# Kernel optimization log

Hardware: AMD Instinct MI355X
Metric: run time of the kernel (lower is better)

## Reference

```python
import jax, jax.numpy as jnp
import numpy as np

B, N, D = 16, 1024, 768
H = 12
HD = D // H           # 64
NUM_BUCKETS = 49      # iRPE 'product' buckets, shared across heads
SCALE = HD ** -0.5


def setup_inputs() -> dict:
    key = jax.random.key(0)
    k1, k2, k3, k4, k5, k6 = jax.random.split(key, 6)
    x = jax.random.normal(k1, (B, N, D), dtype=jnp.float32)
    qkv_w = jax.random.normal(k2, (3 * D, D), dtype=jnp.float32) * 0.02
    rpe_table = jax.random.normal(k3, (NUM_BUCKETS, HD), dtype=jnp.float32) * 0.02
    rp_bucket = jax.random.randint(k4, (N, N), 0, NUM_BUCKETS, dtype=jnp.int32)
    proj_w = jax.random.normal(k5, (D, D), dtype=jnp.float32) * 0.02
    proj_b = jax.random.normal(k6, (D,), dtype=jnp.float32) * 0.02
    return {"x": x, "qkv_w": qkv_w, "rpe_table": rpe_table,
            "rp_bucket": rp_bucket, "proj_w": proj_w, "proj_b": proj_b}


def reference(x, qkv_w, rpe_table, rp_bucket, proj_w, proj_b):
    b, n, d = x.shape
    # qkv projection (no bias), split into q,k,v of shape [B,H,N,HD]
    qkv = (x @ qkv_w.T).reshape(b, n, 3, H, HD)
    qkv = jnp.transpose(qkv, (2, 0, 3, 1, 4))
    q, k, v = qkv[0], qkv[1], qkv[2]
    q = q * SCALE
    # full attention scores [B,H,N,N]
    attn = jnp.einsum('bhid,bhjd->bhij', q, k)
    # iRPE contextual bias on keys: project q onto the bucket table, then
    # gather per relative-position bucket: bias[b,h,i,j] = (q @ W^T)[b,h,i,rp_bucket[i,j]]
    bias_all = jnp.einsum('bhid,cd->bhic', q, rpe_table)   # [B,H,N,num_buckets]
    bias = bias_all[:, :, jnp.arange(n)[:, None], rp_bucket]  # [B,H,N,N]
    attn = jax.nn.softmax(attn + bias, axis=-1)
    out = jnp.einsum('bhij,bhjd->bhid', attn, v)            # [B,H,N,HD]
    out = jnp.transpose(out, (0, 2, 1, 3)).reshape(b, n, d)
    return out @ proj_w.T + proj_b
```

## Files before the change

### kernel.cpp

```cpp
#include <hip/hip_runtime.h>

typedef short bf16x8 __attribute__((ext_vector_type(8)));
typedef float f32x4 __attribute__((ext_vector_type(4)));

#define QSCALE 0.1803368801111204f

__device__ __forceinline__ unsigned short f2bf(float f){
  unsigned u = __float_as_uint(f);
  u = (u + 0x7fffu + ((u >> 16) & 1u)) >> 16;
  return (unsigned short)u;
}
__device__ __forceinline__ f32x4 mfma16(bf16x8 a, bf16x8 b, f32x4 c){
  return __builtin_amdgcn_mfma_f32_16x16x32_bf16(a, b, c, 0, 0, 0);
}
__device__ __forceinline__ void gload_lds16(const void* g, void* l){
  __builtin_amdgcn_global_load_lds((__attribute__((address_space(1))) void*)(g),
                                   (__attribute__((address_space(3))) void*)(l), 16, 0, 0);
}
__device__ __forceinline__ unsigned cvt_pk_bf16(float lo, float hi){
  unsigned r;
  asm("v_cvt_pk_bf16_f32 %0, %1, %2" : "=v"(r) : "v"(lo), "v"(hi));
  return r;
}
__device__ __forceinline__ float exp2_fast(float x){
  float r;
  asm("v_exp_f32 %0, %1" : "=v"(r) : "v"(x));
  return r;
}

__global__ __launch_bounds__(256) void prep_kernel(
    const float* __restrict__ x, const float* __restrict__ qw,
    const float* __restrict__ pw, const int* __restrict__ rp,
    unsigned short* __restrict__ xb, unsigned short* __restrict__ wb,
    unsigned short* __restrict__ pwb, unsigned char* __restrict__ rp8){
  const int T1 = 3145728;
  const int T2 = T1 + 442368;
  const int T3 = T2 + 147456;
  const int T4 = T3 + 262144;
  for (int t = blockIdx.x * 256 + threadIdx.x; t < T4; t += gridDim.x * 256){
    if (t < T3){
      const float4* src; ushort4* dst; int off;
      if (t < T1){ src = (const float4*)x;  dst = (ushort4*)xb;  off = t; }
      else if (t < T2){ src = (const float4*)qw; dst = (ushort4*)wb;  off = t - T1; }
      else { src = (const float4*)pw; dst = (ushort4*)pwb; off = t - T2; }
      float4 v = src[off];
      ushort4 u;
      u.x = f2bf(v.x); u.y = f2bf(v.y); u.z = f2bf(v.z); u.w = f2bf(v.w);
      dst[off] = u;
    } else {
      int off = t - T3;
      int4 v = ((const int4*)rp)[off];
      int row = (off * 4) >> 10;
      int sw = (row & 7) << 4;
      uchar4 u;
      u.x = (unsigned char)((v.x << 1) ^ sw);
      u.y = (unsigned char)((v.y << 1) ^ sw);
      u.z = (unsigned char)((v.z << 1) ^ sw);
      u.w = (unsigned char)((v.w << 1) ^ sw);
      ((uchar4*)rp8)[off] = u;
    }
  }
}

__device__ __forceinline__ void gemm_core(
    const unsigned short* __restrict__ A, const unsigned short* __restrict__ Bm,
    int m0, int n0, int K, unsigned short* As, unsigned short* Bs,
    f32x4 (&acc)[4][4]){
  const int tid = threadIdx.x, lane = tid & 63, wave = tid >> 6;
  const int g = lane >> 4, r16 = lane & 15;
  const int wr = wave >> 1, wc = wave & 1;
  for (int k0 = 0; k0 < K; k0 += 32){
    __syncthreads();
    #pragma unroll
    for (int j = 0; j < 2; j++){
      int ci = j * 256 + tid;
      int row = ci >> 2, c = ci & 3;
      gload_lds16(A  + (size_t)(m0 + row) * K + k0 + c * 8,
                  (char*)As + (j * 256 + wave * 64) * 16);
      gload_lds16(Bm + (size_t)(n0 + row) * K + k0 + c * 8,
                  (char*)Bs + (j * 256 + wave * 64) * 16);
    }
    __syncthreads();
    bf16x8 a[4], b[4];
    #pragma unroll
    for (int mi = 0; mi < 4; mi++)
      a[mi] = *(const bf16x8*)((const char*)As + (wr * 64 + mi * 16 + r16) * 64 + g * 16);
    #pragma unroll
    for (int ni = 0; ni < 4; ni++)
      b[ni] = *(const bf16x8*)((const char*)Bs + (wc * 64 + ni * 16 + r16) * 64 + g * 16);
    #pragma unroll
    for (int mi = 0; mi < 4; mi++)
      #pragma unroll
      for (int ni = 0; ni < 4; ni++)
        acc[mi][ni] = mfma16(b[ni], a[mi], acc[mi][ni]);
  }
}

__global__ __launch_bounds__(256) void qkv_gemm(
    const unsigned short* __restrict__ xb, const unsigned short* __restrict__ wb,
    unsigned short* __restrict__ q_s, unsigned short* __restrict__ k_s,
    unsigned short* __restrict__ v_t){
  __shared__ __align__(16) unsigned short As[128 * 32];
  __shared__ __align__(16) unsigned short Bs[128 * 32];
  f32x4 acc[4][4];
  #pragma unroll
  for (int i = 0; i < 4; i++)
    #pragma unroll
    for (int j = 0; j < 4; j++){
      acc[i][j][0] = 0.f; acc[i][j][1] = 0.f; acc[i][j][2] = 0.f; acc[i][j][3] = 0.f;
    }
  const int m0 = blockIdx.y * 128, n0 = blockIdx.x * 128;
  gemm_core(xb, wb, m0, n0, 768, As, Bs, acc);

  const int lane = threadIdx.x & 63, wave = threadIdx.x >> 6;
  const int g = lane >> 4, r16 = lane & 15;
  const int wr = wave >> 1, wc = wave & 1;
  const int sel = n0 / 768;
  #pragma unroll
  for (int mi = 0; mi < 4; mi++){
    int grow = m0 + wr * 64 + mi * 16 + r16;
    int bb = grow >> 10, ii = grow & 1023;
    #pragma unroll
    for (int ni = 0; ni < 4; ni++){
      int gcol0 = n0 + wc * 64 + ni * 16 + 4 * g;
      int rem = gcol0 - sel * 768;
      int h = rem >> 6, hd0 = rem & 63;
      size_t base = ((size_t)(bb * 12 + h)) << 16;
      f32x4 v = acc[mi][ni];
      if (sel == 0){
        ushort4 u;
        u.x = f2bf(v[0] * QSCALE); u.y = f2bf(v[1] * QSCALE);
        u.z = f2bf(v[2] * QSCALE); u.w = f2bf(v[3] * QSCALE);
        *(ushort4*)(q_s + base + ((size_t)ii << 6) + hd0) = u;
      } else if (sel == 1){
        ushort4 u;
        u.x = f2bf(v[0]); u.y = f2bf(v[1]); u.z = f2bf(v[2]); u.w = f2bf(v[3]);
        *(ushort4*)(k_s + base + ((size_t)ii << 6) + hd0) = u;
      } else {
        #pragma unroll
        for (int r = 0; r < 4; r++)
          v_t[base + ((size_t)(hd0 + r) << 10) + ii] = f2bf(v[r]);
      }
    }
  }
}

__global__ __launch_bounds__(256) void attn_kernel(
    const unsigned short* __restrict__ q_s, const unsigned short* __restrict__ k_s,
    const unsigned short* __restrict__ v_t, const unsigned char* __restrict__ rp8,
    const float* __restrict__ rpe, unsigned short* __restrict__ ao){
  __shared__ __align__(16) char smem[32768];
  const int tid = threadIdx.x, lane = tid & 63, w = tid >> 6;
  const int g = lane >> 4, r16 = lane & 15;
  const int qb = blockIdx.x, bh = blockIdx.y;
  const size_t bh_base = (size_t)bh << 16;

  const int i_loc = w * 16 + r16;
  const size_t qoff = bh_base + ((size_t)(qb * 64 + i_loc) << 6);
  bf16x8 qf0 = *(const bf16x8*)(q_s + qoff + g * 8);
  bf16x8 qf1 = *(const bf16x8*)(q_s + qoff + 32 + g * 8);

  char* bias_lds = smem + 24576;
  const int s16 = (r16 & 7) << 4;
  #pragma unroll
  for (int jt = 0; jt < 4; jt++){
    int crow = jt * 16 + r16;
    bf16x8 a0, a1;
    #pragma unroll
    for (int e = 0; e < 8; e++){ a0[e] = 0; a1[e] = 0; }
    if (crow < 49){
      const float* rr = rpe + crow * 64 + g * 8;
      float4 x0 = *(const float4*)(rr);
      float4 x1 = *(const float4*)(rr + 4);
      float4 y0 = *(const float4*)(rr + 32);
      float4 y1 = *(const float4*)(rr + 36);
      a0[0]=f2bf(x0.x); a0[1]=f2bf(x0.y); a0[2]=f2bf(x0.z); a0[3]=f2bf(x0.w);
      a0[4]=f2bf(x1.x); a0[5]=f2bf(x1.y); a0[6]=f2bf(x1.z); a0[7]=f2bf(x1.w);
      a1[0]=f2bf(y0.x); a1[1]=f2bf(y0.y); a1[2]=f2bf(y0.z); a1[3]=f2bf(y0.w);
      a1[4]=f2bf(y1.x); a1[5]=f2bf(y1.y); a1[6]=f2bf(y1.z); a1[7]=f2bf(y1.w);
    }
    f32x4 z = {0.f, 0.f, 0.f, 0.f};
    z = mfma16(a0, qf0, z);
    z = mfma16(a1, qf1, z);
    uint2 u; u.x = cvt_pk_bf16(z[0], z[1]); u.y = cvt_pk_bf16(z[2], z[3]);
    *(uint2*)(bias_lds + i_loc * 128 + ((jt * 32 + 8 * g) ^ s16)) = u;
  }

  unsigned short* ks = (unsigned short*)smem;
  unsigned short* vs = (unsigned short*)(smem + 8192);
  char* pbuf = smem + 16384 + w * 2048;
  const char* browb = bias_lds + i_loc * 128;

  const int ci0 = tid, ci1 = 256 + tid;
  const int row0 = ci0 >> 3, sc0 = (ci0 & 7) ^ (row0 & 7);
  const int row1 = ci1 >> 3, sc1 = (ci1 & 7) ^ (row1 & 7);
  const char* kp0 = (const char*)(k_s + bh_base) + row0 * 128 + sc0 * 16;
  const char* kp1 = (const char*)(k_s + bh_base) + row1 * 128 + sc1 * 16;
  const char* vp0 = (const char*)(v_t + bh_base) + row0 * 2048 + sc0 * 16;
  const char* vp1 = (const char*)(v_t + bh_base) + row1 * 2048 + sc1 * 16;
  char* kl0 = (char*)smem + w * 1024;
  char* kl1 = (char*)smem + 4096 + w * 1024;
  char* vl0 = (char*)smem + 8192 + w * 1024;
  char* vl1 = (char*)smem + 12288 + w * 1024;
  const unsigned char* rprow = rp8 + ((size_t)(qb * 64 + i_loc) << 10);

  f32x4 o[4];
  #pragma unroll
  for (int dt = 0; dt < 4; dt++){ o[dt][0]=0.f; o[dt][1]=0.f; o[dt][2]=0.f; o[dt][3]=0.f; }
  float m_i = -INFINITY, l_i = 0.f;

  for (int kb = 0; kb < 16; kb++){
    __syncthreads();
    gload_lds16(kp0, kl0);
    gload_lds16(kp1, kl1);
    gload_lds16(vp0, vl0);
    gload_lds16(vp1, vl1);
    kp0 += 8192; kp1 += 8192; vp0 += 128; vp1 += 128;
    __syncthreads();

    f32x4 st[4];
    #pragma unroll
    for (int jt = 0; jt < 4; jt++){
      int krow = jt * 16 + r16;
      int sw = (krow & 7) << 4;
      bf16x8 ka0 = *(const bf16x8*)((char*)ks + krow * 128 + ((g * 16) ^ sw));
      bf16x8 ka1 = *(const bf16x8*)((char*)ks + krow * 128 + ((64 + g * 16) ^ sw));
      f32x4 z = {0.f, 0.f, 0.f, 0.f};
      z = mfma16(ka0, qf0, z);
      z = mfma16(ka1, qf1, z);
      st[jt] = z;
    }
    #pragma unroll
    for (int jt = 0; jt < 4; jt++){
      unsigned bu = *(const unsigned*)(rprow + kb * 64 + jt * 16 + g * 4);
      st[jt][0] += __uint_as_float((unsigned)*(const unsigned short*)(browb + (bu & 0xff)) << 16);
      st[jt][1] += __uint_as_float((unsigned)*(const unsigned short*)(browb + ((bu >> 8) & 0xff)) << 16);
      st[jt][2] += __uint_as_float((unsigned)*(const unsigned short*)(browb + ((bu >> 16) & 0xff)) << 16);
      st[jt][3] += __uint_as_float((unsigned)*(const unsigned short*)(browb + (bu >> 24)) << 16);
    }
    float tmax = -INFINITY;
    #pragma unroll
    for (int jt = 0; jt < 4; jt++)
      tmax = fmaxf(tmax, fmaxf(fmaxf(st[jt][0], st[jt][1]), fmaxf(st[jt][2], st[jt][3])));
    tmax = fmaxf(tmax, __shfl_xor(tmax, 16));
    tmax = fmaxf(tmax, __shfl_xor(tmax, 32));
    const bool skip = __all(tmax <= m_i + 8.f);
    if (!skip){
      float mnew = fmaxf(m_i, tmax);
      float alpha = exp2_fast(m_i - mnew);
      m_i = mnew;
      l_i *= alpha;
      float af[4];
      #pragma unroll
      for (int r = 0; r < 4; r++) af[r] = __shfl(alpha, 4 * g + r);
      #pragma unroll
      for (int dt = 0; dt < 4; dt++){
        o[dt][0] *= af[0]; o[dt][1] *= af[1]; o[dt][2] *= af[2]; o[dt][3] *= af[3];
      }
    }
    #pragma unroll
    for (int jt = 0; jt < 4; jt++){
      float p0 = exp2_fast(st[jt][0] - m_i);
      float p1 = exp2_fast(st[jt][1] - m_i);
      float p2 = exp2_fast(st[jt][2] - m_i);
      float p3 = exp2_fast(st[jt][3] - m_i);
      l_i += (p0 + p1) + (p2 + p3);
      uint2 u; u.x = cvt_pk_bf16(p0, p1); u.y = cvt_pk_bf16(p2, p3);
      *(uint2*)(pbuf + r16 * 128 + ((jt * 32 + g * 8) ^ ((r16 & 7) << 4))) = u;
    }
    #pragma unroll
    for (int kt = 0; kt < 2; kt++){
      bf16x8 pa = *(const bf16x8*)(pbuf + r16 * 128 + ((kt * 64 + g * 16) ^ ((r16 & 7) << 4)));
      #pragma unroll
      for (int dt = 0; dt < 4; dt++){
        int vrow = dt * 16 + r16;
        bf16x8 vb = *(const bf16x8*)((char*)vs + vrow * 128 + ((kt * 64 + g * 16) ^ ((vrow & 7) << 4)));
        o[dt] = mfma16(pa, vb, o[dt]);
      }
    }
  }

  l_i += __shfl_xor(l_i, 16);
  l_i += __shfl_xor(l_i, 32);
  float lf[4];
  #pragma unroll
  for (int r = 0; r < 4; r++) lf[r] = 1.f / __shfl(l_i, 4 * g + r);
  const int bidx = bh / 12, h = bh - bidx * 12;
  #pragma unroll
  for (int dt = 0; dt < 4; dt++){
    int d = dt * 16 + r16;
    #pragma unroll
    for (int r = 0; r < 4; r++){
      int i = qb * 64 + w * 16 + 4 * g + r;
      ao[(size_t)(bidx * 1024 + i) * 768 + h * 64 + d] = f2bf(o[dt][r] * lf[r]);
    }
  }
}

__global__ __launch_bounds__(256) void proj_gemm(
    const unsigned short* __restrict__ aob, const unsigned short* __restrict__ pwb,
    const float* __restrict__ pb, float* __restrict__ out){
  __shared__ __align__(16) unsigned short As[128 * 32];
  __shared__ __align__(16) unsigned short Bs[128 * 32];
  f32x4 acc[4][4];
  #pragma unroll
  for (int i = 0; i < 4; i++)
    #pragma unroll
    for (int j = 0; j < 4; j++){
      acc[i][j][0] = 0.f; acc[i][j][1] = 0.f; acc[i][j][2] = 0.f; acc[i][j][3] = 0.f;
    }
  const int m0 = blockIdx.y * 128, n0 = blockIdx.x * 128;
  gemm_core(aob, pwb, m0, n0, 768, As, Bs, acc);

  const int lane = threadIdx.x & 63, wave = threadIdx.x >> 6;
  const int g = lane >> 4, r16 = lane & 15;
  const int wr = wave >> 1, wc = wave & 1;
  #pragma unroll
  for (int mi = 0; mi < 4; mi++){
    int grow = m0 + wr * 64 + mi * 16 + r16;
    #pragma unroll
    for (int ni = 0; ni < 4; ni++){
      int gcol0 = n0 + wc * 64 + ni * 16 + 4 * g;
      float4 b4 = *(const float4*)(pb + gcol0);
      f32x4 v = acc[mi][ni];
      float4 ov;
      ov.x = v[0] + b4.x; ov.y = v[1] + b4.y;
      ov.z = v[2] + b4.z; ov.w = v[3] + b4.w;
      *(float4*)(out + (size_t)grow * 768 + gcol0) = ov;
    }
  }
}

extern "C" void kernel_launch(void* const* d_in, const int* in_sizes, int n_in,
                              void* d_out, int out_size, void* d_ws, size_t ws_size,
                              hipStream_t stream){
  const float* x      = (const float*)d_in[0];
  const float* qkv_w  = (const float*)d_in[1];
  const float* rpe    = (const float*)d_in[2];
  const int*   rp     = (const int*)d_in[3];
  const float* proj_w = (const float*)d_in[4];
  const float* proj_b = (const float*)d_in[5];
  float* out = (float*)d_out;
  char* ws = (char*)d_ws;

  unsigned short* xb  = (unsigned short*)(ws);
  unsigned short* wb  = (unsigned short*)(ws + 25165824);
  unsigned short* pwb = (unsigned short*)(ws + 28704768);
  unsigned char*  rp8 = (unsigned char*) (ws + 29884416);
  unsigned short* q_s = (unsigned short*)(ws + 30932992);
  unsigned short* k_s = (unsigned short*)(ws + 56098816);
  unsigned short* v_t = (unsigned short*)(ws + 81264640);
  unsigned short* aob = (unsigned short*)(ws + 106430464);

  prep_kernel<<<2048, 256, 0, stream>>>(x, qkv_w, proj_w, rp, xb, wb, pwb, rp8);
  qkv_gemm<<<dim3(18, 128), 256, 0, stream>>>(xb, wb, q_s, k_s, v_t);
  attn_kernel<<<dim3(16, 192), 256, 0, stream>>>(q_s, k_s, v_t, rp8, rpe, aob);
  proj_gemm<<<dim3(6, 128), 256, 0, stream>>>(aob, pwb, proj_b, out);
}
```

Measured before the change: 299.6 us.

## Use 256x256 double-buffered swizzled GEMM tiles for QKV and projection

Replaces the 128x128 single-buffered GEMM core with a 256x256 tile, 512-thread version that double-buffers A and B in 64KB of LDS, using XOR-swizzled layouts and staged async global-to-LDS loads interleaved with MFMA quads. It targets the per-k-step double-sync stalls and low arithmetic intensity of the old GEMMs. The cost is fewer blocks (576 for QKV, 192 for projection), which may underfill the device, especially for the projection. Register pressure rises with 32 accumulators per wave.

Measured after the change: 281.4 us. -6.1%, faster.

```diff
diff --git a/kernel.cpp b/kernel.cpp
--- a/kernel.cpp
+++ b/kernel.cpp
@@ -62,63 +62,112 @@
   }
 }
 
-__device__ __forceinline__ void gemm_core(
+__device__ __forceinline__ void stage_half256(
+    const unsigned short* __restrict__ M, int r0, int K, int kt, int half,
+    char* dst, int tid){
+  int ci = half * 512 + tid;
+  int lr = ci >> 3, s = ci & 7;
+  int cc = s ^ (lr & 7);
+  int grow = lr * 2 + (cc >> 2);
+  int gk = (cc & 3) * 8;
+  gload_lds16(M + (size_t)(r0 + grow) * K + kt * 32 + gk, dst + ci * 16);
+}
+
+__device__ __forceinline__ void gemm_core256(
     const unsigned short* __restrict__ A, const unsigned short* __restrict__ Bm,
-    int m0, int n0, int K, unsigned short* As, unsigned short* Bs,
-    f32x4 (&acc)[4][4]){
-  const int tid = threadIdx.x, lane = tid & 63, wave = tid >> 6;
-  const int g = lane >> 4, r16 = lane & 15;
-  const int wr = wave >> 1, wc = wave & 1;
-  for (int k0 = 0; k0 < K; k0 += 32){
-    __syncthreads();
-    #pragma unroll
-    for (int j = 0; j < 2; j++){
-      int ci = j * 256 + tid;
-      int row = ci >> 2, c = ci & 3;
-      gload_lds16(A  + (size_t)(m0 + row) * K + k0 + c * 8,
-                  (char*)As + (j * 256 + wave * 64) * 16);
-      gload_lds16(Bm + (size_t)(n0 + row) * K + k0 + c * 8,
-                  (char*)Bs + (j * 256 + wave * 64) * 16);
-    }
-    __syncthreads();
-    bf16x8 a[4], b[4];
-    #pragma unroll
-    for (int mi = 0; mi < 4; mi++)
-      a[mi] = *(const bf16x8*)((const char*)As + (wr * 64 + mi * 16 + r16) * 64 + g * 16);
-    #pragma unroll
-    for (int ni = 0; ni < 4; ni++)
-      b[ni] = *(const bf16x8*)((const char*)Bs + (wc * 64 + ni * 16 + r16) * 64 + g * 16);
-    #pragma unroll
-    for (int mi = 0; mi < 4; mi++)
-      #pragma unroll
-      for (int ni = 0; ni < 4; ni++)
-        acc[mi][ni] = mfma16(b[ni], a[mi], acc[mi][ni]);
-  }
-}
-
-__global__ __launch_bounds__(256) void qkv_gemm(
+    int m0, int n0, int K, char* smem, f32x4 (&acc)[8][4]){
+  const int tid = threadIdx.x, lane = tid & 63;
+  const int w = tid >> 6, g = lane >> 4, r16 = lane & 15;
+  const int wr = w >> 2, wc = w & 3;
+  const int NT = K >> 5;
+  char* Ab0 = smem;            char* Ab1 = smem + 16384;
+  char* Bb0 = smem + 32768;    char* Bb1 = smem + 49152;
+
+  stage_half256(Bm, n0, K, 0, 0, Bb0, tid);
+  stage_half256(Bm, n0, K, 0, 1, Bb0, tid);
+  stage_half256(A,  m0, K, 0, 0, Ab0, tid);
+  stage_half256(A,  m0, K, 0, 1, Ab0, tid);
+  stage_half256(Bm, n0, K, 1, 0, Bb1, tid);
+  stage_half256(Bm, n0, K, 1, 1, Bb1, tid);
+
+  const int arb = wr * 128 + r16;
+  const int brb = wc * 64 + r16;
+  bf16x8 bq[4];
+
+#define LOADB_(buf) { \
+  _Pragma("unroll") \
+  for (int ni = 0; ni < 4; ni++){ \
+    int row = brb + ni * 16; int lr = row >> 1; \
+    bq[ni] = *(const bf16x8*)((buf) + lr * 128 + ((((row & 1) << 6) + g * 16) ^ ((lr & 7) << 4))); } }
+#define QUAD_(buf, p) { \
+  int ra = arb + (2 * (p)) * 16; int rb = ra + 16; \
+  int la = ra >> 1, lb = rb >> 1; \
+  bf16x8 afa = *(const bf16x8*)((buf) + la * 128 + ((((ra & 1) << 6) + g * 16) ^ ((la & 7) << 4))); \
+  bf16x8 afb = *(const bf16x8*)((buf) + lb * 128 + ((((rb & 1) << 6) + g * 16) ^ ((lb & 7) << 4))); \
+  _Pragma("unroll") \
+  for (int ni = 0; ni < 4; ni++){ \
+    acc[2 * (p)][ni]     = mfma16(bq[ni], afa, acc[2 * (p)][ni]); \
+    acc[2 * (p) + 1][ni] = mfma16(bq[ni], afb, acc[2 * (p) + 1][ni]); } }
+
+  for (int T = 0; T < NT; T += 2){
+    int t2 = T + 2, t3 = T + 3;
+    if (t2 >= NT) t2 -= NT;
+    if (t3 >= NT) t3 -= NT;
+    asm volatile("s_waitcnt vmcnt(2) lgkmcnt(0)" ::: "memory");
+    __builtin_amdgcn_s_barrier();
+    __builtin_amdgcn_sched_barrier(0);
+    stage_half256(A, m0, K, T + 1, 0, Ab1, tid);
+    LOADB_(Bb0); QUAD_(Ab0, 0);
+    stage_half256(A, m0, K, T + 1, 1, Ab1, tid);
+    QUAD_(Ab0, 1);
+    asm volatile("s_waitcnt lgkmcnt(0)" ::: "memory");
+    __builtin_amdgcn_s_barrier();
+    __builtin_amdgcn_sched_barrier(0);
+    stage_half256(Bm, n0, K, t2, 0, Bb0, tid);
+    QUAD_(Ab0, 2);
+    stage_half256(Bm, n0, K, t2, 1, Bb0, tid);
+    QUAD_(Ab0, 3);
+    asm volatile("s_waitcnt vmcnt(2) lgkmcnt(0)" ::: "memory");
+    __builtin_amdgcn_s_barrier();
+    __builtin_amdgcn_sched_barrier(0);
+    stage_half256(A, m0, K, t2, 0, Ab0, tid);
+    LOADB_(Bb1); QUAD_(Ab1, 0);
+    stage_half256(A, m0, K, t2, 1, Ab0, tid);
+    QUAD_(Ab1, 1);
+    asm volatile("s_waitcnt lgkmcnt(0)" ::: "memory");
+    __builtin_amdgcn_s_barrier();
+    __builtin_amdgcn_sched_barrier(0);
+    stage_half256(Bm, n0, K, t3, 0, Bb1, tid);
+    QUAD_(Ab1, 2);
+    stage_half256(Bm, n0, K, t3, 1, Bb1, tid);
+    QUAD_(Ab1, 3);
+  }
+#undef LOADB_
+#undef QUAD_
+}
+
+__global__ __launch_bounds__(512, 2) void qkv_gemm(
     const unsigned short* __restrict__ xb, const unsigned short* __restrict__ wb,
     unsigned short* __restrict__ q_s, unsigned short* __restrict__ k_s,
     unsigned short* __restrict__ v_t){
-  __shared__ __align__(16) unsigned short As[128 * 32];
-  __shared__ __align__(16) unsigned short Bs[128 * 32];
-  f32x4 acc[4][4];
-  #pragma unroll
-  for (int i = 0; i < 4; i++)
+  __shared__ __align__(16) char smem[65536];
+  f32x4 acc[8][4];
+  #pragma unroll
+  for (int i = 0; i < 8; i++)
     #pragma unroll
     for (int j = 0; j < 4; j++){
       acc[i][j][0] = 0.f; acc[i][j][1] = 0.f; acc[i][j][2] = 0.f; acc[i][j][3] = 0.f;
     }
-  const int m0 = blockIdx.y * 128, n0 = blockIdx.x * 128;
-  gemm_core(xb, wb, m0, n0, 768, As, Bs, acc);
-
-  const int lane = threadIdx.x & 63, wave = threadIdx.x >> 6;
+  const int m0 = blockIdx.y * 256, n0 = blockIdx.x * 256;
+  gemm_core256(xb, wb, m0, n0, 768, smem, acc);
+
+  const int tid = threadIdx.x, lane = tid & 63, w = tid >> 6;
   const int g = lane >> 4, r16 = lane & 15;
-  const int wr = wave >> 1, wc = wave & 1;
+  const int wr = w >> 2, wc = w & 3;
   const int sel = n0 / 768;
   #pragma unroll
-  for (int mi = 0; mi < 4; mi++){
-    int grow = m0 + wr * 64 + mi * 16 + r16;
+  for (int mi = 0; mi < 8; mi++){
+    int grow = m0 + wr * 128 + mi * 16 + r16;
     int bb = grow >> 10, ii = grow & 1023;
     #pragma unroll
     for (int ni = 0; ni < 4; ni++){
@@ -297,27 +346,26 @@
   }
 }
 
-__global__ __launch_bounds__(256) void proj_gemm(
+__global__ __launch_bounds__(512, 2) void proj_gemm(
     const unsigned short* __restrict__ aob, const unsigned short* __restrict__ pwb,
     const float* __restrict__ pb, float* __restrict__ out){
-  __shared__ __align__(16) unsigned short As[128 * 32];
-  __shared__ __align__(16) unsigned short Bs[128 * 32];
-  f32x4 acc[4][4];
-  #pragma unroll
-  for (int i = 0; i < 4; i++)
+  __shared__ __align__(16) char smem[65536];
+  f32x4 acc[8][4];
+  #pragma unroll
+  for (int i = 0; i < 8; i++)
     #pragma unroll
     for (int j = 0; j < 4; j++){
       acc[i][j][0] = 0.f; acc[i][j][1] = 0.f; acc[i][j][2] = 0.f; acc[i][j][3] = 0.f;
     }
-  const int m0 = blockIdx.y * 128, n0 = blockIdx.x * 128;
-  gemm_core(aob, pwb, m0, n0, 768, As, Bs, acc);
-
-  const int lane = threadIdx.x & 63, wave = threadIdx.x >> 6;
+  const int m0 = blockIdx.y * 256, n0 = blockIdx.x * 256;
+  gemm_core256(aob, pwb, m0, n0, 768, smem, acc);
+
+  const int tid = threadIdx.x, lane = tid & 63, w = tid >> 6;
   const int g = lane >> 4, r16 = lane & 15;
-  const int wr = wave >> 1, wc = wave & 1;
-  #pragma unroll
-  for (int mi = 0; mi < 4; mi++){
-    int grow = m0 + wr * 64 + mi * 16 + r16;
+  const int wr = w >> 2, wc = w & 3;
+  #pragma unroll
+  for (int mi = 0; mi < 8; mi++){
+    int grow = m0 + wr * 128 + mi * 16 + r16;
     #pragma unroll
     for (int ni = 0; ni < 4; ni++){
       int gcol0 = n0 + wc * 64 + ni * 16 + 4 * g;
@@ -353,7 +401,7 @@
   unsigned short* aob = (unsigned short*)(ws + 106430464);
 
   prep_kernel<<<2048, 256, 0, stream>>>(x, qkv_w, proj_w, rp, xb, wb, pwb, rp8);
-  qkv_gemm<<<dim3(18, 128), 256, 0, stream>>>(xb, wb, q_s, k_s, v_t);
+  qkv_gemm<<<dim3(9, 64), 512, 0, stream>>>(xb, wb, q_s, k_s, v_t);
   attn_kernel<<<dim3(16, 192), 256, 0, stream>>>(q_s, k_s, v_t, rp8, rpe, aob);
-  proj_gemm<<<dim3(6, 128), 256, 0, stream>>>(aob, pwb, proj_b, out);
-}
+  proj_gemm<<<dim3(3, 64), 512, 0, stream>>>(aob, pwb, proj_b, out);
+}
```
